# Performance work log

Hardware: AMD Instinct MI355X
Metric: run time of the kernel (lower is better)

Reference implementation:

```python
import jax, jax.numpy as jnp
import numpy as np
from jax.scipy.special import erf

F = 64          # scalar feature channels (hidden_irreps multiplicity)
S = 9           # spherical harmonics dim for max_ell=2
NB = 8          # num_bessel
RMAX = 5.0
PPOLY = 5       # num_polynomial_cutoff
AVG_NEIGH = 16.0
SIGMA = 1.0     # atomic_multipoles_smearing_width
KE = 1.0        # Coulomb constant (model units)
N = 20000; G = 20; E = 320000; NEL = 10; L = 2; HMLP = 16

def _sph_l2(u):
    # real spherical harmonics up to l=2, e3nn 'component' normalization,
    # with permute_to_e3nn_convention (y, z, x) ordering for l=1
    x, y, z = u[..., 0], u[..., 1], u[..., 2]
    s3 = 1.7320508075688772; s5 = 2.23606797749979; s15 = 3.872983346207417
    return jnp.stack([jnp.ones_like(x),
                      s3 * y, s3 * z, s3 * x,
                      s15 * x * y, s15 * y * z, 0.5 * s5 * (3.0 * z * z - 1.0),
                      s15 * x * z, 0.5 * s15 * (x * x - y * y)], axis=-1)

def _radial(r):
    # Bessel basis with smooth polynomial cutoff (p = PPOLY)
    n = jnp.arange(1, NB + 1, dtype=r.dtype)
    rb = jnp.sqrt(2.0 / RMAX) * jnp.sin(n * jnp.pi * r[:, None] / RMAX) / r[:, None]
    x = r / RMAX
    p = float(PPOLY)
    u = (1.0 - 0.5 * (p + 1.0) * (p + 2.0) * x**PPOLY
         + p * (p + 2.0) * x**(PPOLY + 1) - 0.5 * p * (p + 1.0) * x**(PPOLY + 2))
    u = jnp.where(x < 1.0, u, 0.0)
    return rb * u[:, None]

def setup_inputs() -> dict:
    key = jax.random.key(0)
    ks = jax.random.split(key, 20)
    Ng = N // G
    species = jax.random.randint(ks[0], (N,), 0, NEL)
    node_attrs = jax.nn.one_hot(species, NEL, dtype=jnp.float32)
    positions = jax.random.uniform(ks[1], (N, 3), dtype=jnp.float32) * 10.0
    g = jax.random.randint(ks[2], (E,), 0, G)
    s_loc = jax.random.randint(ks[3], (E,), 0, Ng)
    off = jax.random.randint(ks[4], (E,), 1, Ng)   # avoid self edges
    r_loc = (s_loc + off) % Ng
    edge_index = jnp.stack([g * Ng + s_loc, g * Ng + r_loc], axis=0)
    batch = jnp.repeat(jnp.arange(G), Ng)
    sc = 0.1
    atomic_energies = jax.random.normal(ks[5], (NEL,)) * sc
    embed_w = jax.random.normal(ks[6], (NEL, F)) * sc
    radial_w1 = jax.random.normal(ks[7], (L, NB, 64)) * 0.3
    radial_b1 = jnp.zeros((L, 64), jnp.float32)
    radial_w2 = jax.random.normal(ks[8], (L, 64, F)) * 0.2
    prod_w = jax.random.normal(ks[9], (L, NEL, F)) * 0.3
    readout_w = jax.random.normal(ks[10], (L, F)) * sc
    ro2_w1 = jax.random.normal(ks[11], (F, HMLP)) * 0.2
    ro2_b1 = jnp.zeros((HMLP,), jnp.float32)
    ro2_w2 = jax.random.normal(ks[12], (HMLP, 1)) * 0.2
    charge_w = jax.random.normal(ks[13], (L, F)) * sc
    flux_w = jax.random.normal(ks[14], (L, NB)) * sc
    formal_charges = jax.random.normal(ks[15], (NEL,)) * 0.5
    return dict(node_attrs=node_attrs, positions=positions, edge_index=edge_index,
                batch=batch, num_graphs=G, atomic_energies=atomic_energies,
                embed_w=embed_w, radial_w1=radial_w1, radial_b1=radial_b1,
                radial_w2=radial_w2, prod_w=prod_w, readout_w=readout_w,
                ro2_w1=ro2_w1, ro2_b1=ro2_b1, ro2_w2=ro2_w2,
                charge_w=charge_w, flux_w=flux_w, formal_charges=formal_charges)

def reference(node_attrs, positions, edge_index, batch, num_graphs,
              atomic_energies, embed_w, radial_w1, radial_b1, radial_w2,
              prod_w, readout_w, ro2_w1, ro2_b1, ro2_w2,
              charge_w, flux_w, formal_charges):
    Nn = node_attrs.shape[0]
    Ng = Nn // num_graphs
    snd, rcv = edge_index[0], edge_index[1]
    # atomic reference energies (E0) and node embedding
    node_e0 = node_attrs @ atomic_energies                      # [N]
    e0 = jax.ops.segment_sum(node_e0, batch, num_graphs)        # [G]
    node_scalars = node_attrs @ embed_w                         # [N,F]
    # edge geometry: gather, spherical harmonics, radial embedding
    vec = positions[rcv] - positions[snd]                       # [E,3]
    lengths = jnp.sqrt((vec * vec).sum(-1) + 1e-12)             # [E]
    unit = vec / lengths[:, None]
    edge_attrs = _sph_l2(unit)                                  # [E,S]
    edge_feats = _radial(lengths)                               # [E,NB]
    # formal charges (per-species)
    FQ = node_attrs @ formal_charges                            # [N]
    charge_density = FQ
    flux = jnp.zeros_like(lengths)
    energies = [e0]
    node_e_list = [node_e0]
    nL = radial_w1.shape[0]
    for l in range(nL):
        # interaction: radial MLP -> per-edge TP messages -> scatter sum
        R = jax.nn.silu(edge_feats @ radial_w1[l] + radial_b1[l]) @ radial_w2[l]  # [E,F]
        m = (R * node_scalars[snd])[:, :, None] * edge_attrs[:, None, :]          # [E,F,S]
        agg = jax.ops.segment_sum(m, rcv, Nn) / AVG_NEIGH                         # [N,F,S]
        # equivariant product (correlation-2 flavor) + element-dependent skip
        sk = node_scalars * (node_attrs @ prod_w[l])                              # [N,F]
        feats = agg + agg * agg[:, :, :1]                                         # [N,F,S]
        node_scalars = feats[:, :, 0] + sk                                        # [N,F]
        if l == nL - 1:
            node_energies = (jax.nn.silu(node_scalars @ ro2_w1 + ro2_b1) @ ro2_w2)[:, 0]
        else:
            node_energies = node_scalars @ readout_w[l]
        energies.append(jax.ops.segment_sum(node_energies, batch, num_graphs))
        node_e_list.append(node_energies)
        # long-range source maps: per-node charge + per-edge flux contributions
        charge_density = charge_density + node_scalars @ charge_w[l]
        flux = flux + edge_feats @ flux_w[l]
    contributions = jnp.stack(energies, -1)                     # [G, L+1]
    total_energy = contributions.sum(-1)                        # [G]
    node_energy = jnp.stack(node_e_list, -1).sum(-1)            # [N]
    # polarization: edge-flux dipole + formal-charge dipole
    pol = jax.ops.segment_sum(flux[:, None] * vec, batch[rcv], num_graphs)
    pol = pol + jax.ops.segment_sum(FQ[:, None] * positions, batch, num_graphs)
    # direct (non-PBC) screened Coulomb energy per graph, equal-size graphs
    q = charge_density.reshape(num_graphs, Ng)
    p = positions.reshape(num_graphs, Ng, 3)
    d = p[:, :, None, :] - p[:, None, :, :]
    r = jnp.sqrt((d * d).sum(-1) + 1e-12)
    kern = erf(r / (2.0 * SIGMA)) / r * (1.0 - jnp.eye(Ng, dtype=r.dtype))
    e_el = 0.5 * KE * jnp.einsum('gi,gij,gj->g', q, kern, q)
    total_energy = total_energy + e_el
    total_charge = jax.ops.segment_sum(charge_density, batch, num_graphs)
    return total_energy, node_energy, contributions, pol, total_charge
```

## Files before the change

kernel.cpp:

```cpp
#include <hip/hip_runtime.h>
#include <math.h>

#define NEL 10
#define FD 64
#define NBES 8
#define GG 20
#define HML 16
#define EGB 1280
#define NUB 5000

typedef __attribute__((ext_vector_type(8))) short short8;
typedef __attribute__((ext_vector_type(4))) float f32x4;

__device__ __forceinline__ float wred(float v) {
    #pragma unroll
    for (int off = 32; off > 0; off >>= 1) v += __shfl_down(v, off, 64);
    return v;
}

__device__ __forceinline__ float silu(float h) {
    return h / (1.f + __expf(-h));
}

__device__ __forceinline__ unsigned short f2bf(float x) {
    unsigned int b = __float_as_uint(x);
    unsigned int r = (b + 0x7FFFu + ((b >> 16) & 1u)) >> 16;
    return (unsigned short)r;
}

__device__ __forceinline__ unsigned int cvt_pk_bf16(float a, float b) {
    unsigned int r;
    asm("v_cvt_pk_bf16_f32 %0, %1, %2" : "=v"(r) : "v"(a), "v"(b));
    return r;
}

__device__ __forceinline__ int xcd_swizzle(int bid, int nb) {
    int q = nb >> 3, r = nb & 7;
    int x = bid & 7, i = bid >> 3;
    return (x < r ? x * (q + 1) : r * (q + 1) + (x - r) * q) + i;
}

__global__ __launch_bounds__(256) void hist_k(
    const int* __restrict__ eidx, int* __restrict__ cnt, int E_)
{
    int e = blockIdx.x * 256 + threadIdx.x;
    atomicAdd(&cnt[eidx[E_ + e]], 1);
}

__global__ __launch_bounds__(1024) void scan_k(
    const int* __restrict__ cnt, int* __restrict__ cur, int N_)
{
    int t = threadIdx.x;
    __shared__ int wtot[16];
    int lane = t & 63, wid = t >> 6;
    int base = t * 20;
    int c[20]; int s = 0;
    bool full = (base + 20 <= N_);
    if (full) {
        #pragma unroll
        for (int i = 0; i < 5; ++i) {
            int4 v4 = *(const int4*)&cnt[base + i * 4];
            c[i*4+0] = v4.x; c[i*4+1] = v4.y; c[i*4+2] = v4.z; c[i*4+3] = v4.w;
        }
        #pragma unroll
        for (int i = 0; i < 20; ++i) s += c[i];
    } else {
        #pragma unroll
        for (int i = 0; i < 20; ++i) { int idx = base + i; c[i] = (idx < N_) ? cnt[idx] : 0; s += c[i]; }
    }
    int v = s;
    #pragma unroll
    for (int off = 1; off < 64; off <<= 1) {
        int u = __shfl_up(v, off, 64);
        if (lane >= off) v += u;
    }
    if (lane == 63) wtot[wid] = v;
    __syncthreads();
    if (wid == 0 && lane < 16) {
        int wv = wtot[lane];
        #pragma unroll
        for (int off = 1; off < 16; off <<= 1) {
            int u = __shfl_up(wv, off, 64);
            if (lane >= off) wv += u;
        }
        wtot[lane] = wv;
    }
    __syncthreads();
    int ex = (wid > 0 ? wtot[wid - 1] : 0) + (v - s);
    if (full) {
        int o[20];
        #pragma unroll
        for (int i = 0; i < 20; ++i) { o[i] = ex; ex += c[i]; }
        #pragma unroll
        for (int i = 0; i < 5; ++i)
            *(int4*)&cur[base + i * 4] = make_int4(o[i*4+0], o[i*4+1], o[i*4+2], o[i*4+3]);
    } else {
        #pragma unroll
        for (int i = 0; i < 20; ++i) {
            int idx = base + i;
            if (idx < N_) { cur[idx] = ex; ex += c[i]; }
        }
    }
}

__global__ __launch_bounds__(256) void setup_geom_k(
    const float* __restrict__ pos, const int* __restrict__ eidx,
    const float* __restrict__ flux_w, int* __restrict__ cur,
    unsigned short* __restrict__ bessel, unsigned int* __restrict__ ids,
    float* __restrict__ polpart,
    const float* __restrict__ attrs, const float* __restrict__ ae,
    const float* __restrict__ fc, const float* __restrict__ embed_w,
    int* __restrict__ spec, float* __restrict__ q, float* __restrict__ out,
    float* __restrict__ scal,
    const float* __restrict__ w1, const float* __restrict__ w2,
    unsigned short* __restrict__ w1bf, unsigned short* __restrict__ w2bf,
    int N_, int E_, int ng)
{
    int bid = blockIdx.x, t = threadIdx.x;
    if (bid < EGB) {
        __shared__ float lpol[GG * 3];
        for (int i = t; i < GG * 3; i += 256) lpol[i] = 0.f;
        __syncthreads();
        int e = bid * 256 + t;
        if (e < E_) {
            float fw[NBES];
            #pragma unroll
            for (int i = 0; i < NBES; ++i) fw[i] = flux_w[i] + flux_w[NBES + i];
            unsigned int magic = (unsigned int)(0xFFFFFFFFull / (unsigned int)ng) + 1u;
            const float PI = 3.14159265358979323846f;
            int s = eidx[e], r = eidx[E_ + e];
            float dx = pos[(size_t)r*3+0] - pos[(size_t)s*3+0];
            float dy = pos[(size_t)r*3+1] - pos[(size_t)s*3+1];
            float dz = pos[(size_t)r*3+2] - pos[(size_t)s*3+2];
            float len = sqrtf(dx*dx + dy*dy + dz*dz + 1e-12f);
            float x = len * 0.2f;
            float u = 0.f;
            if (x < 1.f) {
                float x2 = x * x;
                float x5 = x2 * x2 * x;
                u = 1.f - 21.f * x5 + 35.f * x5 * x - 15.f * x5 * x2;
            }
            float pref = 0.6324555320336759f / len * u;
            float theta = PI * x;
            float s1, c1;
            __sincosf(theta, &s1, &c1);
            float c2 = 2.f * c1;
            float sp_ = 0.f, sn = s1;
            float flux = 0.f;
            unsigned int pk[4];
            #pragma unroll
            for (int i = 0; i < 4; ++i) {
                float r0 = pref * sn;
                float n1 = c2 * sn - sp_; sp_ = sn; sn = n1;
                float r1 = pref * sn;
                n1 = c2 * sn - sp_; sp_ = sn; sn = n1;
                flux += r0 * fw[2*i] + r1 * fw[2*i+1];
                pk[i] = cvt_pk_bf16(r0, r1);
            }
            int p = atomicAdd(&cur[r], 1);
            *(uint4*)&bessel[(size_t)p * NBES] = make_uint4(pk[0], pk[1], pk[2], pk[3]);
            ids[p] = (unsigned int)s | ((unsigned int)r << 16);
            int g = (int)__umulhi((unsigned int)r, magic);
            atomicAdd(&lpol[g*3+0], flux * dx);
            atomicAdd(&lpol[g*3+1], flux * dy);
            atomicAdd(&lpol[g*3+2], flux * dz);
        }
        __syncthreads();
        for (int i = t; i < GG * 3; i += 256) polpart[bid * (GG * 3) + i] = lpol[i];
    } else if (bid < EGB + 36) {
        int idx = (bid - EGB) * 256 + t;
        if (idx < 8192) {
            int l = idx >> 12, rem = idx & 4095;
            int f = rem >> 6, k = rem & 63;
            w2bf[idx] = f2bf(w2[l * 4096 + k * 64 + f]);
        } else {
            int j = idx - 8192;
            int l = j >> 9, rem = j & 511;
            int mm = rem >> 3, jj = rem & 7;
            w1bf[j] = f2bf(w1[l * 512 + jj * 64 + mm]);
        }
        if (idx < GG) out[idx] = 0.f;
    } else {
        int idx = (bid - (EGB + 36)) * 256 + t;
        int lane = t & 63;
        int n = idx >> 6;
        bool pred = (lane < NEL) && (attrs[(size_t)n * NEL + lane] > 0.5f);
        unsigned long long m = __ballot(pred);
        int sp = (int)__builtin_ctzll(m);
        scal[idx] = embed_w[sp * FD + lane];
        if (lane == 0) { spec[n] = sp; q[n] = fc[sp]; out[GG + n] = ae[sp]; }
    }
}

__global__ __launch_bounds__(256, 4) void edge_mlp_k(
    const unsigned short* __restrict__ bessel, const unsigned int* __restrict__ ids,
    const unsigned short* __restrict__ w1bf, const float* __restrict__ b1,
    const unsigned short* __restrict__ w2bf, const float* __restrict__ scal,
    float* __restrict__ agg0, int layer, int E_)
{
    __shared__ __align__(16) char smem[4][4352];
    int t = threadIdx.x, w = t >> 6, lane = t & 63;
    int mrow = lane & 15, quad = lane >> 4;
    int xb = xcd_swizzle(blockIdx.x, gridDim.x);
    int wbase = (xb * 4 + w) * 64;
    unsigned short* hw = (unsigned short*)smem[w];
    float* cw = (float*)smem[w];

    unsigned int ids_all = ids[wbase + lane];
    int firstR = (int)(__builtin_amdgcn_readlane(ids_all, 0) >> 16);

    const short8 z8 = {0,0,0,0,0,0,0,0};
    short8 a1f[4];
    #pragma unroll
    for (int nt = 0; nt < 4; ++nt) {
        a1f[nt] = z8;
        if (quad == 0) a1f[nt] = *(const short8*)&w1bf[layer * 512 + (nt * 16 + mrow) * 8];
        else if (quad == 1) a1f[nt][0] = (short)f2bf(b1[layer * FD + nt * 16 + mrow]);
    }
    const unsigned short* wb = w2bf + layer * 4096;
    short8 bf0[4], bf1[4];
    #pragma unroll
    for (int nt = 0; nt < 4; ++nt) {
        bf0[nt] = *(const short8*)&wb[(nt * 16 + mrow) * 64 + quad * 8];
        bf1[nt] = *(const short8*)&wb[(nt * 16 + mrow) * 64 + 32 + quad * 8];
    }

    f32x4 zf = {0.f, 0.f, 0.f, 0.f};
    int curR = firstR;
    float run = 0.f;

    #pragma unroll 1
    for (int grp = 0; grp < 4; ++grp) {
        int ebase = wbase + grp * 16;

        short8 b_ef = z8;
        if (quad == 0) b_ef = *(const short8*)&bessel[(size_t)(ebase + mrow) * NBES];
        else if (quad == 1) b_ef[0] = (short)0x3F80;

        #pragma unroll
        for (int nt = 0; nt < 4; ++nt) {
            f32x4 c1 = __builtin_amdgcn_mfma_f32_16x16x32_bf16(a1f[nt], b_ef, zf, 0, 0, 0);
            unsigned int p01 = cvt_pk_bf16(silu(c1[0]), silu(c1[1]));
            unsigned int p23 = cvt_pk_bf16(silu(c1[2]), silu(c1[3]));
            *(uint2*)&hw[mrow * 72 + nt * 16 + quad * 4] = make_uint2(p01, p23);
        }

        short8 a0  = *(const short8*)&hw[mrow * 72 + quad * 8];
        short8 a1b = *(const short8*)&hw[mrow * 72 + 32 + quad * 8];
        f32x4 c[4];
        #pragma unroll
        for (int nt = 0; nt < 4; ++nt) {
            f32x4 cc = __builtin_amdgcn_mfma_f32_16x16x32_bf16(a0, bf0[nt], zf, 0, 0, 0);
            cc = __builtin_amdgcn_mfma_f32_16x16x32_bf16(a1b, bf1[nt], cc, 0, 0, 0);
            c[nt] = cc;
        }
        #pragma unroll
        for (int nt = 0; nt < 4; ++nt)
            #pragma unroll
            for (int reg = 0; reg < 4; ++reg)
                cw[(quad * 4 + reg) * 68 + nt * 16 + mrow] = c[nt][reg];

        #pragma unroll
        for (int half = 0; half < 2; ++half) {
            float cv[8], sw[8];
            unsigned int idv[8];
            #pragma unroll
            for (int k = 0; k < 8; ++k) {
                int pp = half * 8 + k;
                cv[k] = cw[pp * 68 + lane];
                idv[k] = __builtin_amdgcn_readlane(ids_all, grp * 16 + pp);
                sw[k] = scal[(size_t)(idv[k] & 0xffffu) * FD + lane];
            }
            #pragma unroll
            for (int k = 0; k < 8; ++k) {
                int r = (int)(idv[k] >> 16);
                float v = cv[k] * sw[k];
                if (r != curR) {
                    float* dst = &agg0[(size_t)curR * FD + lane];
                    if (curR != firstR) *dst = run;
                    else atomicAdd(dst, run);
                    run = v; curR = r;
                } else {
                    run += v;
                }
            }
        }
    }
    atomicAdd(&agg0[(size_t)curR * FD + lane], run);
}

__global__ __launch_bounds__(256) void node_update_k(
    float* __restrict__ scal, float* __restrict__ agg0,
    const int* __restrict__ spec, const float* __restrict__ prod_w,
    const float* __restrict__ readout_w, const float* __restrict__ ro2_w1,
    const float* __restrict__ ro2_b1, const float* __restrict__ ro2_w2,
    const float* __restrict__ charge_w, float* __restrict__ q,
    float* __restrict__ out_nodeE, float* __restrict__ nEpart,
    int layer, int last, int N_)
{
    __shared__ float vsh[4][FD];
    __shared__ float red[4];
    int wid = threadIdx.x >> 6, lane = threadIdx.x & 63;
    int n = blockIdx.x * 4 + wid;
    int sp = spec[n];
    size_t idx = (size_t)n * FD + lane;
    float a = agg0[idx] * 0.0625f;
    if (!last) agg0[idx] = 0.f;
    float v = a + a * a + scal[idx] * prod_w[(layer * NEL + sp) * FD + lane];
    scal[idx] = v;

    float ne;
    if (!last) {
        ne = wred(v * readout_w[layer * FD + lane]);
    } else {
        vsh[wid][lane] = v;
        int l16 = lane & 15, qq = lane >> 4;
        float hp = 0.f;
        #pragma unroll
        for (int ff = 0; ff < 16; ++ff) {
            int fidx = qq * 16 + ff;
            hp += vsh[wid][fidx] * ro2_w1[fidx * HML + l16];
        }
        hp += __shfl_down(hp, 32, 64);
        hp += __shfl_down(hp, 16, 64);
        float h = 0.f;
        if (lane < HML) h = silu(ro2_b1[lane] + hp) * ro2_w2[lane];
        ne = wred(h);
    }
    float qs = wred(v * charge_w[layer * FD + lane]);
    if (lane == 0) {
        out_nodeE[n] += ne;
        q[n] += qs;
        red[wid] = ne;
    }
    __syncthreads();
    if (threadIdx.x == 0) nEpart[layer * NUB + blockIdx.x] = red[0] + red[1] + red[2] + red[3];
}

__global__ __launch_bounds__(256) void coulomb_final_k(
    const float* __restrict__ q, const float* __restrict__ pos,
    const int* __restrict__ spec, const float* __restrict__ ae,
    const float* __restrict__ fc, const float* __restrict__ nEpart,
    const float* __restrict__ polpart, float* __restrict__ out,
    int N_, int ng)
{
    __shared__ float sh[260];
    int vb = blockIdx.x;
    int g = vb / 137, rem = vb % 137;
    int t = threadIdx.x, lane = t & 63, w = t >> 6;

    if (rem < 136) {
        int a = 0, r2 = rem;
        while (r2 >= 16 - a) { r2 -= 16 - a; ++a; }
        int b = a + r2;
        const float* qg = q + (size_t)g * ng;
        const float* pg = pos + (size_t)g * ng * 3;
        float* qs_ = sh; float* jx = sh + 64; float* jy = sh + 128; float* jz = sh + 192;
        if (t < 64) {
            int j = b * 64 + t;
            bool ok = j < ng;
            qs_[t] = ok ? qg[j] : 0.f;
            jx[t] = ok ? pg[(size_t)j*3+0] : 0.f;
            jy[t] = ok ? pg[(size_t)j*3+1] : 0.f;
            jz[t] = ok ? pg[(size_t)j*3+2] : 0.f;
        }
        __syncthreads();
        int i = a * 64 + lane;
        float accu = 0.f;
        if (i < ng) {
            float qi = qg[i];
            float xi = pg[(size_t)i*3+0], yi = pg[(size_t)i*3+1], zi = pg[(size_t)i*3+2];
            #pragma unroll 4
            for (int k = 0; k < 16; ++k) {
                int jj = w * 16 + k;
                int j = b * 64 + jj;
                float dx = xi - jx[jj], dy = yi - jy[jj], dz = zi - jz[jj];
                float d2 = dx*dx + dy*dy + dz*dz + 1e-12f;
                float rinv = __frsqrt_rn(d2);
                float r = d2 * rinv;
                float x = 0.5f * r;
                float tt = __frcp_rn(1.f + 0.3275911f * x);
                float poly = ((((1.061405429f*tt - 1.453152027f)*tt + 1.421413741f)*tt
                               - 0.284496736f)*tt + 0.254829592f)*tt;
                float erfv = 1.f - poly * __expf(-x * x);
                float kern = (j == i) ? 0.f : erfv * rinv;
                accu += qi * qs_[jj] * kern;
            }
        }
        accu = wred(accu);
        if (lane == 0) sh[256 + w] = accu;
        __syncthreads();
        if (t == 0) {
            float s = sh[256] + sh[257] + sh[258] + sh[259];
            atomicAdd(&out[g], (a == b) ? 0.5f * s : s);
        }
    } else {
        float se0 = 0.f, sq = 0.f, p0 = 0.f, p1 = 0.f, p2 = 0.f, s0 = 0.f, s1 = 0.f;
        for (int n = g * ng + t; n < (g + 1) * ng; n += 256) {
            int sp = spec[n];
            float fq = fc[sp];
            se0 += ae[sp];
            sq += q[n];
            p0 += fq * pos[(size_t)n*3+0];
            p1 += fq * pos[(size_t)n*3+1];
            p2 += fq * pos[(size_t)n*3+2];
        }
        if (t < 250) {
            int b = g * 250 + t;
            s0 = nEpart[b];
            s1 = nEpart[NUB + b];
        }
        for (int b = t; b < EGB; b += 256) {
            p0 += polpart[b * (GG * 3) + g * 3 + 0];
            p1 += polpart[b * (GG * 3) + g * 3 + 1];
            p2 += polpart[b * (GG * 3) + g * 3 + 2];
        }
        float vals[7] = {se0, s0, s1, sq, p0, p1, p2};
        float* red = sh;
        #pragma unroll
        for (int k = 0; k < 7; ++k) {
            float r = wred(vals[k]);
            if (lane == 0) red[w * 8 + k] = r;
        }
        __syncthreads();
        if (t < 7) sh[64 + t] = red[t] + red[8 + t] + red[16 + t] + red[24 + t];
        __syncthreads();
        if (t == 0) {
            float a0 = sh[64], a1 = sh[65], a2 = sh[66];
            atomicAdd(&out[g], a0 + a1 + a2);
            float* contrib = out + GG + N_;
            contrib[g*3+0] = a0; contrib[g*3+1] = a1; contrib[g*3+2] = a2;
            float* pol = contrib + GG * 3;
            pol[g*3+0] = sh[68]; pol[g*3+1] = sh[69]; pol[g*3+2] = sh[70];
            float* qt = pol + GG * 3;
            qt[g] = sh[67];
        }
    }
}

extern "C" void kernel_launch(void* const* d_in, const int* in_sizes, int n_in,
                              void* d_out, int out_size, void* d_ws, size_t ws_size,
                              hipStream_t stream)
{
    const float* node_attrs      = (const float*)d_in[0];
    const float* positions       = (const float*)d_in[1];
    const int*   edge_index      = (const int*)d_in[2];
    const float* atomic_energies = (const float*)d_in[5];
    const float* embed_w         = (const float*)d_in[6];
    const float* radial_w1       = (const float*)d_in[7];
    const float* radial_b1       = (const float*)d_in[8];
    const float* radial_w2       = (const float*)d_in[9];
    const float* prod_w          = (const float*)d_in[10];
    const float* readout_w       = (const float*)d_in[11];
    const float* ro2_w1          = (const float*)d_in[12];
    const float* ro2_b1          = (const float*)d_in[13];
    const float* ro2_w2          = (const float*)d_in[14];
    const float* charge_w        = (const float*)d_in[15];
    const float* flux_w          = (const float*)d_in[16];
    const float* formal_charges  = (const float*)d_in[17];

    int N = in_sizes[0] / NEL;
    int E = in_sizes[2] / 2;
    int ng = N / GG;

    float* ws      = (float*)d_ws;
    float* scal    = ws;
    float* agg0    = scal + (size_t)N * FD;
    int*   cnt     = (int*)(agg0 + (size_t)N * FD);
    int*   cur     = cnt + N;
    unsigned short* bessel = (unsigned short*)(cur + N);
    unsigned int*   ids    = (unsigned int*)(bessel + (size_t)E * NBES);
    float* q       = (float*)(ids + E);
    int*   spec    = (int*)(q + N);
    float* nEpart  = (float*)(spec + N);
    float* polpart = nEpart + 2 * NUB;
    unsigned short* w2bf = (unsigned short*)(polpart + EGB * (GG * 3));
    unsigned short* w1bf = w2bf + 8192;

    float* out = (float*)d_out;
    float* out_nodeE = out + GG;

    hipMemsetAsync(agg0, 0, ((size_t)N * FD + N) * sizeof(float), stream);

    hist_k<<<E / 256, 256, 0, stream>>>(edge_index, cnt, E);
    scan_k<<<1, 1024, 0, stream>>>(cnt, cur, N);
    setup_geom_k<<<EGB + 36 + (N * FD) / 256, 256, 0, stream>>>(
        positions, edge_index, flux_w, cur, bessel, ids, polpart,
        node_attrs, atomic_energies, formal_charges, embed_w,
        spec, q, out, scal, radial_w1, radial_w2, w1bf, w2bf, N, E, ng);

    for (int l = 0; l < 2; ++l) {
        edge_mlp_k<<<E / 256, 256, 0, stream>>>(
            bessel, ids, w1bf, radial_b1, w2bf, scal, agg0, l, E);
        node_update_k<<<N / 4, 256, 0, stream>>>(
            scal, agg0, spec, prod_w, readout_w, ro2_w1, ro2_b1, ro2_w2,
            charge_w, q, out_nodeE, nEpart, l, (l == 1) ? 1 : 0, N);
    }

    coulomb_final_k<<<GG * 137, 256, 0, stream>>>(
        q, positions, spec, atomic_energies, formal_charges,
        nEpart, polpart, out, N, ng);
}
```

Before: 243.6 us.

## Replace per-edge radial MLP with interpolated lookup table over edge length

Precomputes the radial MLP output for each layer on a uniform grid of edge lengths in the setup kernel, and stores edge records as (ids, length). The edge kernel then linearly interpolates the table instead of recomputing Bessel features and running two MFMA layers per edge. This removes the per-edge matrix work and the bessel buffer, at the cost of extra gathered table reads per edge and an interpolation approximation error.

```diff
diff --git a/kernel.cpp b/kernel.cpp
--- a/kernel.cpp
+++ b/kernel.cpp
@@ -8,6 +8,10 @@
 #define HML 16
 #define EGB 1280
 #define NUB 5000
+#define TKNOT 4096
+#define TROWS 4097
+#define TPAD  4100
+#define TBLK  2049
 
 typedef __attribute__((ext_vector_type(8))) short short8;
 typedef __attribute__((ext_vector_type(4))) float f32x4;
@@ -20,18 +24,6 @@
 
 __device__ __forceinline__ float silu(float h) {
     return h / (1.f + __expf(-h));
-}
-
-__device__ __forceinline__ unsigned short f2bf(float x) {
-    unsigned int b = __float_as_uint(x);
-    unsigned int r = (b + 0x7FFFu + ((b >> 16) & 1u)) >> 16;
-    return (unsigned short)r;
-}
-
-__device__ __forceinline__ unsigned int cvt_pk_bf16(float a, float b) {
-    unsigned int r;
-    asm("v_cvt_pk_bf16_f32 %0, %1, %2" : "=v"(r) : "v"(a), "v"(b));
-    return r;
 }
 
 __device__ __forceinline__ int xcd_swizzle(int bid, int nb) {
@@ -106,17 +98,17 @@
 __global__ __launch_bounds__(256) void setup_geom_k(
     const float* __restrict__ pos, const int* __restrict__ eidx,
     const float* __restrict__ flux_w, int* __restrict__ cur,
-    unsigned short* __restrict__ bessel, unsigned int* __restrict__ ids,
-    float* __restrict__ polpart,
+    uint2* __restrict__ recs, float* __restrict__ polpart,
     const float* __restrict__ attrs, const float* __restrict__ ae,
     const float* __restrict__ fc, const float* __restrict__ embed_w,
     int* __restrict__ spec, float* __restrict__ q, float* __restrict__ out,
     float* __restrict__ scal,
-    const float* __restrict__ w1, const float* __restrict__ w2,
-    unsigned short* __restrict__ w1bf, unsigned short* __restrict__ w2bf,
+    const float* __restrict__ w1, const float* __restrict__ b1,
+    const float* __restrict__ w2, float* __restrict__ tab,
     int N_, int E_, int ng)
 {
     int bid = blockIdx.x, t = threadIdx.x;
+    const float PI = 3.14159265358979323846f;
     if (bid < EGB) {
         __shared__ float lpol[GG * 3];
         for (int i = t; i < GG * 3; i += 256) lpol[i] = 0.f;
@@ -127,7 +119,6 @@
             #pragma unroll
             for (int i = 0; i < NBES; ++i) fw[i] = flux_w[i] + flux_w[NBES + i];
             unsigned int magic = (unsigned int)(0xFFFFFFFFull / (unsigned int)ng) + 1u;
-            const float PI = 3.14159265358979323846f;
             int s = eidx[e], r = eidx[E_ + e];
             float dx = pos[(size_t)r*3+0] - pos[(size_t)s*3+0];
             float dy = pos[(size_t)r*3+1] - pos[(size_t)s*3+1];
@@ -147,19 +138,14 @@
             float c2 = 2.f * c1;
             float sp_ = 0.f, sn = s1;
             float flux = 0.f;
-            unsigned int pk[4];
             #pragma unroll
-            for (int i = 0; i < 4; ++i) {
-                float r0 = pref * sn;
+            for (int i = 0; i < NBES; ++i) {
+                flux += pref * sn * fw[i];
                 float n1 = c2 * sn - sp_; sp_ = sn; sn = n1;
-                float r1 = pref * sn;
-                n1 = c2 * sn - sp_; sp_ = sn; sn = n1;
-                flux += r0 * fw[2*i] + r1 * fw[2*i+1];
-                pk[i] = cvt_pk_bf16(r0, r1);
             }
             int p = atomicAdd(&cur[r], 1);
-            *(uint4*)&bessel[(size_t)p * NBES] = make_uint4(pk[0], pk[1], pk[2], pk[3]);
-            ids[p] = (unsigned int)s | ((unsigned int)r << 16);
+            recs[p] = make_uint2((unsigned int)s | ((unsigned int)r << 16),
+                                 __float_as_uint(len));
             int g = (int)__umulhi((unsigned int)r, magic);
             atomicAdd(&lpol[g*3+0], flux * dx);
             atomicAdd(&lpol[g*3+1], flux * dy);
@@ -167,21 +153,46 @@
         }
         __syncthreads();
         for (int i = t; i < GG * 3; i += 256) polpart[bid * (GG * 3) + i] = lpol[i];
-    } else if (bid < EGB + 36) {
-        int idx = (bid - EGB) * 256 + t;
-        if (idx < 8192) {
-            int l = idx >> 12, rem = idx & 4095;
-            int f = rem >> 6, k = rem & 63;
-            w2bf[idx] = f2bf(w2[l * 4096 + k * 64 + f]);
-        } else {
-            int j = idx - 8192;
-            int l = j >> 9, rem = j & 511;
-            int mm = rem >> 3, jj = rem & 7;
-            w1bf[j] = f2bf(w1[l * 512 + jj * 64 + mm]);
-        }
-        if (idx < GG) out[idx] = 0.f;
+    } else if (bid < EGB + TBLK) {
+        if (bid == EGB && t < GG) out[t] = 0.f;
+        int widg = (bid - EGB) * 4 + (t >> 6);
+        if (widg < 2 * TROWS) {
+            int l = widg / TROWS;
+            int kk = widg - l * TROWS;
+            int f = t & 63;
+            float len = fmaxf((float)kk * (5.f / (float)TKNOT), 1e-6f);
+            float x = len * 0.2f;
+            float u = 0.f;
+            if (x < 1.f) {
+                float x2 = x * x;
+                float x5 = x2 * x2 * x;
+                u = 1.f - 21.f * x5 + 35.f * x5 * x - 15.f * x5 * x2;
+            }
+            float pref = 0.6324555320336759f / len * u;
+            float theta = PI * x;
+            float s1, c1;
+            __sincosf(theta, &s1, &c1);
+            float c2 = 2.f * c1;
+            float sp_ = 0.f, sn = s1;
+            float ef[NBES];
+            #pragma unroll
+            for (int i = 0; i < NBES; ++i) {
+                ef[i] = pref * sn;
+                float n1 = c2 * sn - sp_; sp_ = sn; sn = n1;
+            }
+            float h = b1[l * FD + f];
+            #pragma unroll
+            for (int j = 0; j < NBES; ++j)
+                h = fmaf(ef[j], w1[l * 512 + j * 64 + f], h);
+            h = silu(h);
+            float o = 0.f;
+            #pragma unroll
+            for (int m = 0; m < 64; ++m)
+                o = fmaf(__shfl(h, m, 64), w2[(size_t)l * 4096 + m * 64 + f], o);
+            tab[((size_t)l * TPAD + kk) * 64 + f] = o;
+        }
     } else {
-        int idx = (bid - (EGB + 36)) * 256 + t;
+        int idx = (bid - (EGB + TBLK)) * 256 + t;
         int lane = t & 63;
         int n = idx >> 6;
         bool pred = (lane < NEL) && (attrs[(size_t)n * NEL + lane] > 0.5f);
@@ -193,96 +204,57 @@
 }
 
 __global__ __launch_bounds__(256, 4) void edge_mlp_k(
-    const unsigned short* __restrict__ bessel, const unsigned int* __restrict__ ids,
-    const unsigned short* __restrict__ w1bf, const float* __restrict__ b1,
-    const unsigned short* __restrict__ w2bf, const float* __restrict__ scal,
-    float* __restrict__ agg0, int layer, int E_)
-{
-    __shared__ __align__(16) char smem[4][4352];
+    const uint2* __restrict__ recs, const float* __restrict__ tab,
+    const float* __restrict__ scal, float* __restrict__ agg0, int layer, int E_)
+{
     int t = threadIdx.x, w = t >> 6, lane = t & 63;
-    int mrow = lane & 15, quad = lane >> 4;
     int xb = xcd_swizzle(blockIdx.x, gridDim.x);
     int wbase = (xb * 4 + w) * 64;
-    unsigned short* hw = (unsigned short*)smem[w];
-    float* cw = (float*)smem[w];
-
-    unsigned int ids_all = ids[wbase + lane];
-    int firstR = (int)(__builtin_amdgcn_readlane(ids_all, 0) >> 16);
-
-    const short8 z8 = {0,0,0,0,0,0,0,0};
-    short8 a1f[4];
-    #pragma unroll
-    for (int nt = 0; nt < 4; ++nt) {
-        a1f[nt] = z8;
-        if (quad == 0) a1f[nt] = *(const short8*)&w1bf[layer * 512 + (nt * 16 + mrow) * 8];
-        else if (quad == 1) a1f[nt][0] = (short)f2bf(b1[layer * FD + nt * 16 + mrow]);
-    }
-    const unsigned short* wb = w2bf + layer * 4096;
-    short8 bf0[4], bf1[4];
-    #pragma unroll
-    for (int nt = 0; nt < 4; ++nt) {
-        bf0[nt] = *(const short8*)&wb[(nt * 16 + mrow) * 64 + quad * 8];
-        bf1[nt] = *(const short8*)&wb[(nt * 16 + mrow) * 64 + 32 + quad * 8];
-    }
-
-    f32x4 zf = {0.f, 0.f, 0.f, 0.f};
+    const float* tb = tab + (size_t)layer * TPAD * 64;
+
+    uint2 rec = recs[wbase + lane];
+    float ln = __uint_as_float(rec.y);
+    float tt = ln * ((float)TKNOT / 5.f);
+    int k0l = min((int)tt, TKNOT - 1);
+    float frl = fminf(tt - (float)k0l, 1.f);
+    int offl = k0l * 64;
+
+    int firstR = (int)(__builtin_amdgcn_readlane(rec.x, 0) >> 16);
     int curR = firstR;
     float run = 0.f;
 
     #pragma unroll 1
     for (int grp = 0; grp < 4; ++grp) {
-        int ebase = wbase + grp * 16;
-
-        short8 b_ef = z8;
-        if (quad == 0) b_ef = *(const short8*)&bessel[(size_t)(ebase + mrow) * NBES];
-        else if (quad == 1) b_ef[0] = (short)0x3F80;
-
-        #pragma unroll
-        for (int nt = 0; nt < 4; ++nt) {
-            f32x4 c1 = __builtin_amdgcn_mfma_f32_16x16x32_bf16(a1f[nt], b_ef, zf, 0, 0, 0);
-            unsigned int p01 = cvt_pk_bf16(silu(c1[0]), silu(c1[1]));
-            unsigned int p23 = cvt_pk_bf16(silu(c1[2]), silu(c1[3]));
-            *(uint2*)&hw[mrow * 72 + nt * 16 + quad * 4] = make_uint2(p01, p23);
-        }
-
-        short8 a0  = *(const short8*)&hw[mrow * 72 + quad * 8];
-        short8 a1b = *(const short8*)&hw[mrow * 72 + 32 + quad * 8];
-        f32x4 c[4];
-        #pragma unroll
-        for (int nt = 0; nt < 4; ++nt) {
-            f32x4 cc = __builtin_amdgcn_mfma_f32_16x16x32_bf16(a0, bf0[nt], zf, 0, 0, 0);
-            cc = __builtin_amdgcn_mfma_f32_16x16x32_bf16(a1b, bf1[nt], cc, 0, 0, 0);
-            c[nt] = cc;
-        }
-        #pragma unroll
-        for (int nt = 0; nt < 4; ++nt)
-            #pragma unroll
-            for (int reg = 0; reg < 4; ++reg)
-                cw[(quad * 4 + reg) * 68 + nt * 16 + mrow] = c[nt][reg];
-
-        #pragma unroll
-        for (int half = 0; half < 2; ++half) {
-            float cv[8], sw[8];
-            unsigned int idv[8];
-            #pragma unroll
-            for (int k = 0; k < 8; ++k) {
-                int pp = half * 8 + k;
-                cv[k] = cw[pp * 68 + lane];
-                idv[k] = __builtin_amdgcn_readlane(ids_all, grp * 16 + pp);
-                sw[k] = scal[(size_t)(idv[k] & 0xffffu) * FD + lane];
-            }
-            #pragma unroll
-            for (int k = 0; k < 8; ++k) {
-                int r = (int)(idv[k] >> 16);
-                float v = cv[k] * sw[k];
-                if (r != curR) {
-                    float* dst = &agg0[(size_t)curR * FD + lane];
-                    if (curR != firstR) *dst = run;
-                    else atomicAdd(dst, run);
-                    run = v; curR = r;
-                } else {
-                    run += v;
-                }
+        unsigned int idv[16];
+        int off[16];
+        float fr[16];
+        #pragma unroll
+        for (int k = 0; k < 16; ++k) {
+            int pp = grp * 16 + k;
+            idv[k] = __builtin_amdgcn_readlane(rec.x, pp);
+            off[k] = __builtin_amdgcn_readlane(offl, pp);
+            fr[k]  = __uint_as_float((unsigned int)__builtin_amdgcn_readlane(
+                         __float_as_uint(frl), pp));
+        }
+        float ra[16], rb[16], sw[16];
+        #pragma unroll
+        for (int k = 0; k < 16; ++k) {
+            ra[k] = tb[off[k] + lane];
+            rb[k] = tb[off[k] + 64 + lane];
+            sw[k] = scal[(size_t)(idv[k] & 0xffffu) * FD + lane];
+        }
+        #pragma unroll
+        for (int k = 0; k < 16; ++k) {
+            int r = (int)(idv[k] >> 16);
+            float R = fmaf(fr[k], rb[k] - ra[k], ra[k]);
+            float v = R * sw[k];
+            if (r != curR) {
+                float* dst = &agg0[(size_t)curR * FD + lane];
+                if (curR != firstR) *dst = run;
+                else atomicAdd(dst, run);
+                run = v; curR = r;
+            } else {
+                run += v;
             }
         }
     }
@@ -468,14 +440,12 @@
     float* agg0    = scal + (size_t)N * FD;
     int*   cnt     = (int*)(agg0 + (size_t)N * FD);
     int*   cur     = cnt + N;
-    unsigned short* bessel = (unsigned short*)(cur + N);
-    unsigned int*   ids    = (unsigned int*)(bessel + (size_t)E * NBES);
-    float* q       = (float*)(ids + E);
+    uint2* recs    = (uint2*)(cur + N);
+    float* q       = (float*)(recs + E);
     int*   spec    = (int*)(q + N);
     float* nEpart  = (float*)(spec + N);
     float* polpart = nEpart + 2 * NUB;
-    unsigned short* w2bf = (unsigned short*)(polpart + EGB * (GG * 3));
-    unsigned short* w1bf = w2bf + 8192;
+    float* tab     = polpart + EGB * (GG * 3);
 
     float* out = (float*)d_out;
     float* out_nodeE = out + GG;
@@ -484,14 +454,14 @@
 
     hist_k<<<E / 256, 256, 0, stream>>>(edge_index, cnt, E);
     scan_k<<<1, 1024, 0, stream>>>(cnt, cur, N);
-    setup_geom_k<<<EGB + 36 + (N * FD) / 256, 256, 0, stream>>>(
-        positions, edge_index, flux_w, cur, bessel, ids, polpart,
+    setup_geom_k<<<EGB + TBLK + (N * FD) / 256, 256, 0, stream>>>(
+        positions, edge_index, flux_w, cur, recs, polpart,
         node_attrs, atomic_energies, formal_charges, embed_w,
-        spec, q, out, scal, radial_w1, radial_w2, w1bf, w2bf, N, E, ng);
+        spec, q, out, scal, radial_w1, radial_b1, radial_w2, tab, N, E, ng);
 
     for (int l = 0; l < 2; ++l) {
         edge_mlp_k<<<E / 256, 256, 0, stream>>>(
-            bessel, ids, w1bf, radial_b1, w2bf, scal, agg0, l, E);
+            recs, tab, scal, agg0, l, E);
         node_update_k<<<N / 4, 256, 0, stream>>>(
             scal, agg0, spec, prod_w, readout_w, ro2_w1, ro2_b1, ro2_w2,
             charge_w, q, out_nodeE, nEpart, l, (l == 1) ? 1 : 0, N);
```

Result: faster. 229.2 us (-5.9%).
